# Kernel tuning notes

Hardware: AMD Instinct MI355X
Metric: run time of the kernel (lower is better)

Reference implementation:

```python
import jax
import jax.numpy as jnp
import numpy as np
from jax import lax

# Model dims (see init_kwargs)
B, C, D, M, L = 16, 64, 128, 16, 3
PROJ, OUT = 64, 1  # projection_size defaults to channels; output_size=1


def _spectral_conv(v, w1, w2, bias):
    """FNO 2D spectral convolution. v: [B,C,D,D]; w1,w2: [C,C,M,M,2] (re/im); bias: [C]."""
    vft = jnp.fft.rfft2(v, norm="backward")            # [B,C,D,D//2+1] complex
    w1c = w1[..., 0] + 1j * w1[..., 1]                   # [C,C,M,M]
    w2c = w2[..., 0] + 1j * w2[..., 1]
    top = jnp.einsum("bixy,ioxy->boxy", vft[:, :, :M, :M], w1c)
    bot = jnp.einsum("bixy,ioxy->boxy", vft[:, :, -M:, :M], w2c)
    out_ft = jnp.zeros_like(vft)
    out_ft = out_ft.at[:, :, :M, :M].set(top).at[:, :, -M:, :M].set(bot)
    out = jnp.fft.irfft2(out_ft, s=(D, D), norm="backward")
    return out + bias[None, :, None, None]               # in_bias


def _rk4(f, z0, ts):
    """Fixed-grid RK4 (torchdiffeq method='rk4'): one step per interval; return final state."""
    def step(z, tp):
        h = tp[1] - tp[0]
        k1 = f(z)
        k2 = f(z + 0.5 * h * k1)
        k3 = f(z + 0.5 * h * k2)
        k4 = f(z + h * k3)
        return z + (h / 6.0) * (k1 + 2.0 * k2 + 2.0 * k3 + k4), None
    pairs = jnp.stack([ts[:-1], ts[1:]], axis=1)         # [T-1, 2]
    zf, _ = lax.scan(step, z0, pairs)
    return zf


def setup_inputs() -> dict:
    key = jax.random.key(0)
    ks = jax.random.split(key, 12)
    scale = 1.0 / C                                       # FNO-style spectral weight scale
    z = jax.random.normal(ks[0], (B, 1, D, D), jnp.float32)
    lift_w = jax.random.normal(ks[1], (C, 1), jnp.float32)
    lift_b = jax.random.normal(ks[2], (C,), jnp.float32) * 0.1
    spec_w1 = jax.random.normal(ks[3], (L, C, C, M, M, 2), jnp.float32) * scale
    spec_w2 = jax.random.normal(ks[4], (L, C, C, M, M, 2), jnp.float32) * scale
    fl_bias = jax.random.normal(ks[5], (L, C), jnp.float32) * 0.1
    p1_w = jax.random.normal(ks[6], (PROJ, C), jnp.float32) / np.sqrt(C)
    p1_b = jax.random.normal(ks[7], (PROJ,), jnp.float32) * 0.1
    p2_w = jax.random.normal(ks[8], (OUT, PROJ), jnp.float32) / np.sqrt(PROJ)
    p2_b = jax.random.normal(ks[9], (OUT,), jnp.float32) * 0.1
    samp_ts = jnp.linspace(0.0, 1.0, 5, dtype=jnp.float32)
    return dict(z=z, lift_w=lift_w, lift_b=lift_b, spec_w1=spec_w1, spec_w2=spec_w2,
                fl_bias=fl_bias, p1_w=p1_w, p1_b=p1_b, p2_w=p2_w, p2_b=p2_b,
                samp_ts=samp_ts)


def reference(z, lift_w, lift_b, spec_w1, spec_w2, fl_bias, p1_w, p1_b, p2_w, p2_b, samp_ts):
    # Lifting: pointwise channel lift 1 -> C
    v = jnp.einsum("bixy,oi->boxy", z, lift_w) + lift_b[None, :, None, None]
    out = v
    # n_layers Fourier layers, each integrated with RK4 over samp_ts; take final time
    for l in range(L):
        f = lambda u, l=l: _spectral_conv(u, spec_w1[l], spec_w2[l], fl_bias[l])
        out = _rk4(f, out, samp_ts)
    # Projection: pointwise C -> PROJ -> OUT
    h = jnp.einsum("bcxy,pc->bpxy", out, p1_w) + p1_b[None, :, None, None]
    out = jnp.einsum("bpxy,op->boxy", h, p2_w) + p2_b[None, :, None, None]
    return out
```

## Files before the change

kernel.cpp:

```cpp
#include <hip/hip_runtime.h>

namespace {

constexpr int kNXI = 33;
constexpr int kNY = 16;
constexpr int kNMODE = kNY * kNXI;
constexpr int kModeBlocks = 529;
constexpr int kFwd1Blocks = 1024;

constexpr int WS_ALPHA = 0;
constexpr int WS_GAMMA = 1;
constexpr int WS_S = 4;
constexpr int WS_ZY = WS_S + kNMODE * 2;
constexpr int WS_T = WS_ZY;

constexpr float kTheta = 0.04908738521234052f;

__device__ __forceinline__ float wave_sum(float v) {
  v += __shfl_xor(v, 1);  v += __shfl_xor(v, 2);  v += __shfl_xor(v, 4);
  v += __shfl_xor(v, 8);  v += __shfl_xor(v, 16); v += __shfl_xor(v, 32);
  return v;
}

__global__ __launch_bounds__(256) void fnde_phase1(
    const float* __restrict__ w1, const float* __restrict__ w2,
    const float* __restrict__ flb, const float* __restrict__ lw,
    const float* __restrict__ lb, const float* __restrict__ ts,
    const float* __restrict__ p1w, const float* __restrict__ p1b,
    const float* __restrict__ p2w, const float* __restrict__ p2b,
    const float* __restrict__ z, float* __restrict__ ws) {
  const int b = blockIdx.x;
  const int t = threadIdx.x;

  if (b >= kModeBlocks) {
    __shared__ float zrow2[2][128], tcf[128], tsnf[128], rre2[2][128], rim2[2][128];
    const int bid = b - kModeBlocks;
    const int r = t >> 7, tt = t & 127;
    const int row = bid * 2 + r;
    const int bb = row >> 7, xs = row & 127;
    if (r == 0) sincosf((float)tt * kTheta, &tsnf[tt], &tcf[tt]);
    zrow2[r][tt] = z[bb * 16384 + xs * 128 + tt];
    __syncthreads();
    int y = tt & 15, part = tt >> 4;
    float sre = 0.f, sim = 0.f;
#pragma clang loop unroll(disable)
    for (int j = 0; j < 16; ++j) {
      int ys = (part << 4) + j;
      int k = (y * ys) & 127;
      float zv = zrow2[r][ys];
      sre += zv * tcf[k];
      sim -= zv * tsnf[k];
    }
    rre2[r][tt] = sre; rim2[r][tt] = sim;
    __syncthreads();
    if (tt < 16) {
      float ar = 0.f, ai = 0.f;
#pragma clang loop unroll(disable)
      for (int pp = 0; pp < 8; ++pp) { ar += rre2[r][(pp << 4) + tt]; ai += rim2[r][(pp << 4) + tt]; }
      int idx = (row * 16 + tt) * 2;
      ws[WS_ZY + idx] = ar; ws[WS_ZY + idx + 1] = ai;
    }
    return;
  }

  const int w = t >> 6, o = t & 63;
  const bool isBias = (b == kModeBlocks - 1);

  int xi = 0, y = 0, m = 0;
  if (!isBias) {
    const int xcd = b & 7, k = b >> 3;
    if (k < 64) { xi = xcd * 4 + (k >> 4); y = k & 15; }
    else        { xi = 32;                 y = xcd * 2 + (k - 64); }
    m = y * kNXI + xi;
    const bool inactive = (y == 0) ? (xi > 16) : (xi == 16);
    if (inactive) {
      if (t == 0) { ws[WS_S + 2 * m] = 0.f; ws[WS_S + 2 * m + 1] = 0.f; }
      return;
    }
  }

  __shared__ float2 ubuf[4][64];
  __shared__ float2 pbuf[2][4][64];

  float q = 0.f;
  if (w == 0) {
#pragma clang loop unroll(disable)
    for (int p = 0; p < 64; ++p) q = fmaf(p2w[p], p1w[p * 64 + o], q);
  }

  float zr = isBias ? lb[o] : lw[o], zi = 0.f;
  ubuf[w][o] = make_float2(zr, zi);

  int pb = 0;

#pragma clang loop unroll(disable)
  for (int l = 0; l < 3; ++l) {
    float2 Wc[16];
    if (isBias) {
      const float* lanep = w1 + o * 512;
#pragma unroll
      for (int j = 0; j < 16; ++j)
        Wc[j] = make_float2(lanep[(size_t)(l * 64 + 16 * w + j) * 32768], 0.f);
    } else if (y >= 1) {
      const float* lanep = ((xi <= 15) ? (w1 + (xi * 16 + y) * 2)
                                       : (w2 + ((xi - 17) * 16 + y) * 2)) + o * 512;
#pragma unroll
      for (int j = 0; j < 16; ++j)
        Wc[j] = *reinterpret_cast<const float2*>(
            lanep + (size_t)(l * 64 + 16 * w + j) * 32768);
    } else {
      const bool hasA = (xi <= 15);
      const float* lanepA = w1 + xi * 32 + o * 512;
      const float* lanepB = (xi >= 1) ? (w2 + (16 - xi) * 32 + o * 512)
                                      : (w1 + o * 512);
#pragma unroll
      for (int j = 0; j < 16; ++j) {
        const size_t ioff = (size_t)(l * 64 + 16 * w + j) * 32768;
        const float2 a = hasA ? *reinterpret_cast<const float2*>(lanepA + ioff)
                              : make_float2(0.f, 0.f);
        const float2 bb2 = *reinterpret_cast<const float2*>(lanepB + ioff);
        Wc[j] = make_float2(0.5f * (a.x + bb2.x), 0.5f * (a.y - bb2.y));
      }
    }
    const float bia = isBias ? flb[l * 64 + o] : 0.f;

#pragma clang loop unroll(disable)
    for (int step = 0; step < 4; ++step) {
      const float h = ts[step + 1] - ts[step];
      float accr = 0.f, acci = 0.f;
#pragma clang loop unroll(disable)
      for (int st = 0; st < 4; ++st) {
        float2 x[16];
#pragma unroll
        for (int jj = 0; jj < 8; ++jj)
          *reinterpret_cast<float4*>(&x[2 * jj]) =
              *reinterpret_cast<const float4*>(&ubuf[w][16 * w + 2 * jj]);
        float pr0 = 0.f, pi0 = 0.f, pr1 = 0.f, pi1 = 0.f;
#pragma unroll
        for (int j = 0; j < 16; j += 2) {
          pr0 = fmaf(Wc[j].x,     x[j].x,     pr0);  pr0 = fmaf(-Wc[j].y,     x[j].y,     pr0);
          pi0 = fmaf(Wc[j].x,     x[j].y,     pi0);  pi0 = fmaf(Wc[j].y,      x[j].x,     pi0);
          pr1 = fmaf(Wc[j + 1].x, x[j + 1].x, pr1);  pr1 = fmaf(-Wc[j + 1].y, x[j + 1].y, pr1);
          pi1 = fmaf(Wc[j + 1].x, x[j + 1].y, pi1);  pi1 = fmaf(Wc[j + 1].y,  x[j + 1].x, pi1);
        }
        pbuf[pb][w][o] = make_float2(pr0 + pr1, pi0 + pi1);
        __syncthreads();
        const float2 q0 = pbuf[pb][0][o], q1 = pbuf[pb][1][o];
        const float2 q2 = pbuf[pb][2][o], q3 = pbuf[pb][3][o];
        const float kr = q0.x + q1.x + q2.x + q3.x + bia;
        const float ki = q0.y + q1.y + q2.y + q3.y;
        const float wsm = (st == 1 || st == 2) ? 2.f : 1.f;
        accr = fmaf(wsm, kr, accr); acci = fmaf(wsm, ki, acci);
        float ur, ui;
        if (st < 3) {
          const float cm = (st < 2) ? 0.5f * h : h;
          ur = fmaf(cm, kr, zr); ui = fmaf(cm, ki, zi);
        } else {
          zr = fmaf(h * (1.f / 6.f), accr, zr);
          zi = fmaf(h * (1.f / 6.f), acci, zi);
          ur = zr; ui = zi;
        }
        ubuf[w][o] = make_float2(ur, ui);
        pb ^= 1;
      }
    }
  }

  if (w == 0) {
    if (isBias) {
      const float g = wave_sum(fmaf(p2w[o], p1b[o], q * zr));
      if (o == 0) ws[WS_GAMMA] = g + p2b[0];
    } else {
      const float sr = wave_sum(q * (zr - lw[o]));
      const float si = wave_sum(q * zi);
      if (o == 0) { ws[WS_S + 2 * m] = sr; ws[WS_S + 2 * m + 1] = si; }
      if (m == 0) {
        const float a = wave_sum(q * lw[o]);
        if (o == 0) ws[WS_ALPHA] = a;
      }
    }
  }
}

__global__ void fnde_mid(float* __restrict__ ws) {
  const int b = blockIdx.x >> 4, y = blockIdx.x & 15;
  const int t = threadIdx.x;
  __shared__ float cr[128], ci[128], tc[128], tsn[128], Sre[kNXI], Sim[kNXI];
  sincosf((float)t * kTheta, &tsn[t], &tc[t]);
  int idx = ((b * 128 + t) * 16 + y) * 2;
  cr[t] = ws[WS_ZY + idx]; ci[t] = ws[WS_ZY + idx + 1];
  __syncthreads();
  if (t < kNXI) {
    int x = (t <= 16) ? t : t + 95;
    float ar = 0.f, ai = 0.f;
    for (int xs = 0; xs < 128; ++xs) {
      int k = (x * xs) & 127;
      float c = tc[k], s = tsn[k];
      ar += cr[xs] * c + ci[xs] * s;
      ai += ci[xs] * c - cr[xs] * s;
    }
    int mm = y * kNXI + t;
    float sr = ws[WS_S + 2 * mm], si = ws[WS_S + 2 * mm + 1];
    Sre[t] = sr * ar - si * ai;
    Sim[t] = sr * ai + si * ar;
  }
  __syncthreads();
  const int xs = t;
  float ar, ai;
  if (y > 0) {
    ar = 0.f; ai = 0.f;
    for (int xj = 0; xj < kNXI; ++xj) {
      int x = (xj <= 16) ? xj : xj + 95;
      int k = (x * xs) & 127;
      float c = tc[k], s = tsn[k];
      ar += Sre[xj] * c - Sim[xj] * s;
      ai += Sre[xj] * s + Sim[xj] * c;
    }
  } else {
    ar = Sre[0]; ai = 0.f;
    for (int xj = 1; xj <= 16; ++xj) {
      int k = (xj * xs) & 127;
      ar += 2.f * (Sre[xj] * tc[k] - Sim[xj] * tsn[k]);
    }
  }
  ws[WS_T + idx] = ar; ws[WS_T + idx + 1] = ai;
}

__global__ void fnde_final(const float* __restrict__ z, const float* __restrict__ ws,
                           float* __restrict__ out) {
  const int bid = blockIdx.x;
  const int b = bid >> 7, xs = bid & 127;
  const int t = threadIdx.x;
  __shared__ float Tre[16], Tim[16], tc[128], tsn[128];
  sincosf((float)t * kTheta, &tsn[t], &tc[t]);
  if (t < 16) {
    int idx = ((b * 128 + xs) * 16 + t) * 2;
    Tre[t] = ws[WS_T + idx]; Tim[t] = ws[WS_T + idx + 1];
  }
  __syncthreads();
  float acc = Tre[0];
  for (int y = 1; y < 16; ++y) {
    int k = (y * t) & 127;
    acc += 2.f * (Tre[y] * tc[k] - Tim[y] * tsn[k]);
  }
  float val = ws[WS_ALPHA] * z[b * 16384 + xs * 128 + t] + ws[WS_GAMMA]
            + acc * (1.f / 16384.f);
  out[b * 16384 + xs * 128 + t] = val;
}

}

extern "C" void kernel_launch(void* const* d_in, const int* in_sizes, int n_in,
                              void* d_out, int out_size, void* d_ws, size_t ws_size,
                              hipStream_t stream) {
  (void)in_sizes; (void)n_in; (void)out_size; (void)ws_size;
  const float* z   = (const float*)d_in[0];
  const float* lw  = (const float*)d_in[1];
  const float* lb  = (const float*)d_in[2];
  const float* w1  = (const float*)d_in[3];
  const float* w2  = (const float*)d_in[4];
  const float* flb = (const float*)d_in[5];
  const float* p1w = (const float*)d_in[6];
  const float* p1b = (const float*)d_in[7];
  const float* p2w = (const float*)d_in[8];
  const float* p2b = (const float*)d_in[9];
  const float* ts  = (const float*)d_in[10];
  float* ws = (float*)d_ws;
  float* out = (float*)d_out;

  fnde_phase1<<<dim3(kModeBlocks + kFwd1Blocks), dim3(256), 0, stream>>>(
      w1, w2, flb, lw, lb, ts, p1w, p1b, p2w, p2b, z, ws);
  fnde_mid<<<dim3(256), dim3(128), 0, stream>>>(ws);
  fnde_final<<<dim3(2048), dim3(128), 0, stream>>>(z, ws, out);
}
```

Before: 97.09 us.

## Pack four modes per 512-thread block and broadcast state via readlane

Restructures the mode-integration blocks so each 512-thread block handles four modes, with two waves per mode each covering 32 input channels instead of four waves of 16. The per-stage shared-memory staging of the state vector is replaced by readlane broadcasts, and the forward row-DFT blocks now process four rows each. The aim is fewer blocks, fewer LDS round-trips and a cheaper reduction (two partials instead of four). In exchange, each thread holds 32 complex weights, which raises register pressure and may lower occupancy. Inactive modes now execute the full integration with dummy indices rather than exiting early.

```diff
diff --git a/kernel.cpp b/kernel.cpp
--- a/kernel.cpp
+++ b/kernel.cpp
@@ -3,10 +3,9 @@
 namespace {
 
 constexpr int kNXI = 33;
-constexpr int kNY = 16;
-constexpr int kNMODE = kNY * kNXI;
-constexpr int kModeBlocks = 529;
-constexpr int kFwd1Blocks = 1024;
+constexpr int kNMODE = 528;
+constexpr int kModeBlk = 133;
+constexpr int kFwd1Blk = 512;
 
 constexpr int WS_ALPHA = 0;
 constexpr int WS_GAMMA = 1;
@@ -16,13 +15,17 @@
 
 constexpr float kTheta = 0.04908738521234052f;
 
+__device__ __forceinline__ float rl(float v, int i) {
+  return __uint_as_float(__builtin_amdgcn_readlane(__float_as_uint(v), i));
+}
+
 __device__ __forceinline__ float wave_sum(float v) {
   v += __shfl_xor(v, 1);  v += __shfl_xor(v, 2);  v += __shfl_xor(v, 4);
   v += __shfl_xor(v, 8);  v += __shfl_xor(v, 16); v += __shfl_xor(v, 32);
   return v;
 }
 
-__global__ __launch_bounds__(256) void fnde_phase1(
+__global__ __launch_bounds__(512) void fnde_phase1(
     const float* __restrict__ w1, const float* __restrict__ w2,
     const float* __restrict__ flb, const float* __restrict__ lw,
     const float* __restrict__ lb, const float* __restrict__ ts,
@@ -32,126 +35,153 @@
   const int b = blockIdx.x;
   const int t = threadIdx.x;
 
-  if (b >= kModeBlocks) {
-    __shared__ float zrow2[2][128], tcf[128], tsnf[128], rre2[2][128], rim2[2][128];
-    const int bid = b - kModeBlocks;
+  if (b >= kModeBlk) {
+    __shared__ float zrow4[4][128], tcf[128], tsnf[128], rre4[4][128], rim4[4][128];
     const int r = t >> 7, tt = t & 127;
-    const int row = bid * 2 + r;
+    const int row = (b - kModeBlk) * 4 + r;
     const int bb = row >> 7, xs = row & 127;
     if (r == 0) sincosf((float)tt * kTheta, &tsnf[tt], &tcf[tt]);
-    zrow2[r][tt] = z[bb * 16384 + xs * 128 + tt];
+    zrow4[r][tt] = z[bb * 16384 + xs * 128 + tt];
     __syncthreads();
-    int y = tt & 15, part = tt >> 4;
+    const int y = tt & 15, part = tt >> 4;
     float sre = 0.f, sim = 0.f;
 #pragma clang loop unroll(disable)
     for (int j = 0; j < 16; ++j) {
-      int ys = (part << 4) + j;
-      int k = (y * ys) & 127;
-      float zv = zrow2[r][ys];
+      const int ys = (part << 4) + j;
+      const int k = (y * ys) & 127;
+      const float zv = zrow4[r][ys];
       sre += zv * tcf[k];
       sim -= zv * tsnf[k];
     }
-    rre2[r][tt] = sre; rim2[r][tt] = sim;
+    rre4[r][tt] = sre; rim4[r][tt] = sim;
     __syncthreads();
     if (tt < 16) {
       float ar = 0.f, ai = 0.f;
 #pragma clang loop unroll(disable)
-      for (int pp = 0; pp < 8; ++pp) { ar += rre2[r][(pp << 4) + tt]; ai += rim2[r][(pp << 4) + tt]; }
-      int idx = (row * 16 + tt) * 2;
+      for (int pp = 0; pp < 8; ++pp) { ar += rre4[r][(pp << 4) + tt]; ai += rim4[r][(pp << 4) + tt]; }
+      const int idx = (row * 16 + tt) * 2;
       ws[WS_ZY + idx] = ar; ws[WS_ZY + idx + 1] = ai;
     }
     return;
   }
 
-  const int w = t >> 6, o = t & 63;
-  const bool isBias = (b == kModeBlocks - 1);
-
-  int xi = 0, y = 0, m = 0;
-  if (!isBias) {
-    const int xcd = b & 7, k = b >> 3;
-    if (k < 64) { xi = xcd * 4 + (k >> 4); y = k & 15; }
-    else        { xi = 32;                 y = xcd * 2 + (k - 64); }
-    m = y * kNXI + xi;
-    const bool inactive = (y == 0) ? (xi > 16) : (xi == 16);
-    if (inactive) {
-      if (t == 0) { ws[WS_S + 2 * m] = 0.f; ws[WS_S + 2 * m + 1] = 0.f; }
-      return;
-    }
-  }
-
-  __shared__ float2 ubuf[4][64];
-  __shared__ float2 pbuf[2][4][64];
+  const int pp = t >> 7;
+  const int w = (t >> 6) & 1;
+  const int o = t & 63;
+  const int base = w * 32;
+  const bool isBiasBlk = (b == kModeBlk - 1);
+
+  __shared__ float2 pbuf[2][4][2][64];
+
+  const float t0 = ts[0], t1 = ts[1], t2 = ts[2], t3 = ts[3], t4 = ts[4];
+  const float h0 = t1 - t0, h1 = t2 - t1, h2 = t3 - t2, h3 = t4 - t3;
 
   float q = 0.f;
-  if (w == 0) {
-#pragma clang loop unroll(disable)
-    for (int p = 0; p < 64; ++p) q = fmaf(p2w[p], p1w[p * 64 + o], q);
-  }
-
-  float zr = isBias ? lb[o] : lw[o], zi = 0.f;
-  ubuf[w][o] = make_float2(zr, zi);
-
-  int pb = 0;
+#pragma clang loop unroll(disable)
+  for (int p = 0; p < 64; ++p) q = fmaf(p2w[p], p1w[p * 64 + o], q);
+
+  int pb = pp & 0;
+  pb = 0;
+
+  if (isBiasBlk) {
+    float e = lb[o];
+    const float* lanep = w1 + o * 512;
+#pragma clang loop unroll(disable)
+    for (int l = 0; l < 3; ++l) {
+      float Wr[32];
+#pragma unroll
+      for (int j = 0; j < 32; ++j)
+        Wr[j] = lanep[(size_t)(l * 64 + base + j) * 32768];
+      const float bia = flb[l * 64 + o];
+#pragma clang loop unroll(disable)
+      for (int step = 0; step < 4; ++step) {
+        const float h = (step == 0) ? h0 : (step == 1) ? h1 : (step == 2) ? h2 : h3;
+        float acc = 0.f;
+        float u = e;
+#pragma clang loop unroll(disable)
+        for (int st = 0; st < 4; ++st) {
+          float p0 = 0.f, p1 = 0.f;
+#pragma unroll
+          for (int j = 0; j < 32; j += 2) {
+            p0 = fmaf(Wr[j],     rl(u, base + j),     p0);
+            p1 = fmaf(Wr[j + 1], rl(u, base + j + 1), p1);
+          }
+          pbuf[pb][pp][w][o].x = p0 + p1;
+          __syncthreads();
+          const float kk = pbuf[pb][pp][0][o].x + pbuf[pb][pp][1][o].x + bia;
+          pb ^= 1;
+          const float wsm = (st == 1 || st == 2) ? 2.f : 1.f;
+          acc = fmaf(wsm, kk, acc);
+          if (st < 3) { const float cm = (st < 2) ? 0.5f * h : h; u = fmaf(cm, kk, e); }
+          else        { e = fmaf(h * (1.f / 6.f), acc, e); u = e; }
+        }
+      }
+    }
+    if (pp == 0 && w == 0) {
+      const float g = wave_sum(fmaf(p2w[o], p1b[o], q * e));
+      if (o == 0) ws[WS_GAMMA] = g + p2b[0];
+    }
+    return;
+  }
+
+  const int kk = b * 4 + pp;
+  const int xi = kk >> 4, y = kk & 15;
+  const int m = y * kNXI + xi;
+  const bool active = !((y == 0 && xi > 16) || (xi == 16 && y > 0));
+  const int xiE = active ? xi : 0;
+  const int yE = active ? y : 1;
+
+  float zr = lw[o], zi = 0.f;
+  float ur = zr, ui = zi;
 
 #pragma clang loop unroll(disable)
   for (int l = 0; l < 3; ++l) {
-    float2 Wc[16];
-    if (isBias) {
-      const float* lanep = w1 + o * 512;
-#pragma unroll
-      for (int j = 0; j < 16; ++j)
-        Wc[j] = make_float2(lanep[(size_t)(l * 64 + 16 * w + j) * 32768], 0.f);
-    } else if (y >= 1) {
-      const float* lanep = ((xi <= 15) ? (w1 + (xi * 16 + y) * 2)
-                                       : (w2 + ((xi - 17) * 16 + y) * 2)) + o * 512;
-#pragma unroll
-      for (int j = 0; j < 16; ++j)
-        Wc[j] = *reinterpret_cast<const float2*>(
-            lanep + (size_t)(l * 64 + 16 * w + j) * 32768);
+    float2 Wc[32];
+    if (yE >= 1) {
+      const float* lanep = ((xiE <= 15) ? (w1 + (xiE * 16 + yE) * 2)
+                                        : (w2 + ((xiE - 17) * 16 + yE) * 2)) + o * 512;
+#pragma unroll
+      for (int j = 0; j < 32; ++j)
+        Wc[j] = *reinterpret_cast<const float2*>(lanep + (size_t)(l * 64 + base + j) * 32768);
     } else {
-      const bool hasA = (xi <= 15);
-      const float* lanepA = w1 + xi * 32 + o * 512;
-      const float* lanepB = (xi >= 1) ? (w2 + (16 - xi) * 32 + o * 512)
-                                      : (w1 + o * 512);
-#pragma unroll
-      for (int j = 0; j < 16; ++j) {
-        const size_t ioff = (size_t)(l * 64 + 16 * w + j) * 32768;
+      const bool hasA = (xiE <= 15);
+      const float* lanepA = w1 + xiE * 32 + o * 512;
+      const float* lanepB = (xiE >= 1) ? (w2 + (16 - xiE) * 32 + o * 512)
+                                       : (w1 + o * 512);
+#pragma unroll
+      for (int j = 0; j < 32; ++j) {
+        const size_t ioff = (size_t)(l * 64 + base + j) * 32768;
         const float2 a = hasA ? *reinterpret_cast<const float2*>(lanepA + ioff)
                               : make_float2(0.f, 0.f);
         const float2 bb2 = *reinterpret_cast<const float2*>(lanepB + ioff);
         Wc[j] = make_float2(0.5f * (a.x + bb2.x), 0.5f * (a.y - bb2.y));
       }
     }
-    const float bia = isBias ? flb[l * 64 + o] : 0.f;
 
 #pragma clang loop unroll(disable)
     for (int step = 0; step < 4; ++step) {
-      const float h = ts[step + 1] - ts[step];
+      const float h = (step == 0) ? h0 : (step == 1) ? h1 : (step == 2) ? h2 : h3;
       float accr = 0.f, acci = 0.f;
 #pragma clang loop unroll(disable)
       for (int st = 0; st < 4; ++st) {
-        float2 x[16];
-#pragma unroll
-        for (int jj = 0; jj < 8; ++jj)
-          *reinterpret_cast<float4*>(&x[2 * jj]) =
-              *reinterpret_cast<const float4*>(&ubuf[w][16 * w + 2 * jj]);
         float pr0 = 0.f, pi0 = 0.f, pr1 = 0.f, pi1 = 0.f;
 #pragma unroll
-        for (int j = 0; j < 16; j += 2) {
-          pr0 = fmaf(Wc[j].x,     x[j].x,     pr0);  pr0 = fmaf(-Wc[j].y,     x[j].y,     pr0);
-          pi0 = fmaf(Wc[j].x,     x[j].y,     pi0);  pi0 = fmaf(Wc[j].y,      x[j].x,     pi0);
-          pr1 = fmaf(Wc[j + 1].x, x[j + 1].x, pr1);  pr1 = fmaf(-Wc[j + 1].y, x[j + 1].y, pr1);
-          pi1 = fmaf(Wc[j + 1].x, x[j + 1].y, pi1);  pi1 = fmaf(Wc[j + 1].y,  x[j + 1].x, pi1);
+        for (int j = 0; j < 32; j += 2) {
+          const float x0r = rl(ur, base + j),     x0i = rl(ui, base + j);
+          const float x1r = rl(ur, base + j + 1), x1i = rl(ui, base + j + 1);
+          pr0 = fmaf(Wc[j].x,     x0r, pr0);  pr0 = fmaf(-Wc[j].y,     x0i, pr0);
+          pi0 = fmaf(Wc[j].x,     x0i, pi0);  pi0 = fmaf(Wc[j].y,      x0r, pi0);
+          pr1 = fmaf(Wc[j + 1].x, x1r, pr1);  pr1 = fmaf(-Wc[j + 1].y, x1i, pr1);
+          pi1 = fmaf(Wc[j + 1].x, x1i, pi1);  pi1 = fmaf(Wc[j + 1].y,  x1r, pi1);
         }
-        pbuf[pb][w][o] = make_float2(pr0 + pr1, pi0 + pi1);
+        pbuf[pb][pp][w][o] = make_float2(pr0 + pr1, pi0 + pi1);
         __syncthreads();
-        const float2 q0 = pbuf[pb][0][o], q1 = pbuf[pb][1][o];
-        const float2 q2 = pbuf[pb][2][o], q3 = pbuf[pb][3][o];
-        const float kr = q0.x + q1.x + q2.x + q3.x + bia;
-        const float ki = q0.y + q1.y + q2.y + q3.y;
+        const float2 qa = pbuf[pb][pp][0][o], qb = pbuf[pb][pp][1][o];
+        pb ^= 1;
+        const float kr = qa.x + qb.x;
+        const float ki = qa.y + qb.y;
         const float wsm = (st == 1 || st == 2) ? 2.f : 1.f;
         accr = fmaf(wsm, kr, accr); acci = fmaf(wsm, ki, acci);
-        float ur, ui;
         if (st < 3) {
           const float cm = (st < 2) ? 0.5f * h : h;
           ur = fmaf(cm, kr, zr); ui = fmaf(cm, ki, zi);
@@ -160,17 +190,12 @@
           zi = fmaf(h * (1.f / 6.f), acci, zi);
           ur = zr; ui = zi;
         }
-        ubuf[w][o] = make_float2(ur, ui);
-        pb ^= 1;
       }
     }
   }
 
   if (w == 0) {
-    if (isBias) {
-      const float g = wave_sum(fmaf(p2w[o], p1b[o], q * zr));
-      if (o == 0) ws[WS_GAMMA] = g + p2b[0];
-    } else {
+    if (active) {
       const float sr = wave_sum(q * (zr - lw[o]));
       const float si = wave_sum(q * zi);
       if (o == 0) { ws[WS_S + 2 * m] = sr; ws[WS_S + 2 * m + 1] = si; }
@@ -178,6 +203,8 @@
         const float a = wave_sum(q * lw[o]);
         if (o == 0) ws[WS_ALPHA] = a;
       }
+    } else {
+      if (o == 0) { ws[WS_S + 2 * m] = 0.f; ws[WS_S + 2 * m + 1] = 0.f; }
     }
   }
 }
@@ -268,7 +295,7 @@
   float* ws = (float*)d_ws;
   float* out = (float*)d_out;
 
-  fnde_phase1<<<dim3(kModeBlocks + kFwd1Blocks), dim3(256), 0, stream>>>(
+  fnde_phase1<<<dim3(kModeBlk + kFwd1Blk), dim3(512), 0, stream>>>(
       w1, w2, flb, lw, lb, ts, p1w, p1b, p2w, p2b, z, ws);
   fnde_mid<<<dim3(256), dim3(128), 0, stream>>>(ws);
   fnde_final<<<dim3(2048), dim3(128), 0, stream>>>(z, ws, out);
```

Result: slower. 185.1 us (+90.6%).

## Split per-mode 3-layer RK4 chain into forward/adjoint halves meeting in the middle

Applied to the files above, without the earlier changes.

Each mode's serial chain of 12 RK4 steps (three layers of four) is split across two blocks. One block propagates the lifted vector forward through layers 0 and 1 (U). The other propagates the projection vector q backward through the transposed layer-2 operator (V). The scalar response is then recovered in the mid kernel as the dot product of V and U, and the bias/gamma term is handled by five small extra blocks. This halves the serial dependency length per block and doubles the block count. In exchange it adds workspace traffic, transposed (strided) weight loads, and redundant per-thread alpha and dot-product loops in the mid kernel.

```diff
diff --git a/kernel.cpp b/kernel.cpp
--- a/kernel.cpp
+++ b/kernel.cpp
@@ -3,38 +3,37 @@
 namespace {
 
 constexpr int kNXI = 33;
-constexpr int kNY = 16;
-constexpr int kNMODE = kNY * kNXI;
-constexpr int kModeBlocks = 529;
-constexpr int kFwd1Blocks = 1024;
-
-constexpr int WS_ALPHA = 0;
-constexpr int WS_GAMMA = 1;
-constexpr int WS_S = 4;
-constexpr int WS_ZY = WS_S + kNMODE * 2;
+constexpr int kNMODE = 528;
+constexpr int kChainBlk = 1061;
+constexpr int kFwd1Blk = 1024;
+
+constexpr int WS_Q = 0;
+constexpr int WS_GAMMA = 64;
+constexpr int WS_ALPHA = 65;
+constexpr int WS_G1 = 68;
+constexpr int WS_G2 = 132;
+constexpr int WS_G3 = 196;
+constexpr int WS_G4 = 260;
+constexpr int WS_G5 = 324;
+constexpr int WS_U = 392;
+constexpr int WS_V = WS_U + kNMODE * 128;
+constexpr int WS_ZY = WS_V + kNMODE * 128;
 constexpr int WS_T = WS_ZY;
 
 constexpr float kTheta = 0.04908738521234052f;
-
-__device__ __forceinline__ float wave_sum(float v) {
-  v += __shfl_xor(v, 1);  v += __shfl_xor(v, 2);  v += __shfl_xor(v, 4);
-  v += __shfl_xor(v, 8);  v += __shfl_xor(v, 16); v += __shfl_xor(v, 32);
-  return v;
-}
 
 __global__ __launch_bounds__(256) void fnde_phase1(
     const float* __restrict__ w1, const float* __restrict__ w2,
     const float* __restrict__ flb, const float* __restrict__ lw,
     const float* __restrict__ lb, const float* __restrict__ ts,
-    const float* __restrict__ p1w, const float* __restrict__ p1b,
-    const float* __restrict__ p2w, const float* __restrict__ p2b,
+    const float* __restrict__ p1w, const float* __restrict__ p2w,
     const float* __restrict__ z, float* __restrict__ ws) {
   const int b = blockIdx.x;
   const int t = threadIdx.x;
 
-  if (b >= kModeBlocks) {
+  if (b >= kChainBlk) {
     __shared__ float zrow2[2][128], tcf[128], tsnf[128], rre2[2][128], rim2[2][128];
-    const int bid = b - kModeBlocks;
+    const int bid = b - kChainBlk;
     const int r = t >> 7, tt = t & 127;
     const int row = bid * 2 + r;
     const int bb = row >> 7, xs = row & 127;
@@ -64,69 +63,89 @@
   }
 
   const int w = t >> 6, o = t & 63;
-  const bool isBias = (b == kModeBlocks - 1);
-
-  int xi = 0, y = 0, m = 0;
-  if (!isBias) {
-    const int xcd = b & 7, k = b >> 3;
+
+  int seg0L = 0, seg0N = 4, seg1L = 1, seg1N = 2;
+  int biasSeg = -1;
+  bool trans = false, herm = false, hasA = true, cplx = true;
+  bool needQ = false, writeQ = false, startLw = false, startLb = false;
+  const float* sA = w1;
+  const float* sB = w1;
+  int outOff = -1;
+
+  if (b < 1056) {
+    const int xcd = b & 7, kk = b >> 3;
+    const int k = kk >> 1, side = kk & 1;
+    int xi, y;
     if (k < 64) { xi = xcd * 4 + (k >> 4); y = k & 15; }
     else        { xi = 32;                 y = xcd * 2 + (k - 64); }
-    m = y * kNXI + xi;
+    const int m = y * kNXI + xi;
     const bool inactive = (y == 0) ? (xi > 16) : (xi == 16);
-    if (inactive) {
-      if (t == 0) { ws[WS_S + 2 * m] = 0.f; ws[WS_S + 2 * m + 1] = 0.f; }
-      return;
-    }
-  }
+    if (inactive) return;
+    herm = (y == 0);
+    if (!herm) {
+      sA = (xi <= 15) ? (w1 + (xi * 16 + y) * 2) : (w2 + ((xi - 17) * 16 + y) * 2);
+    } else {
+      hasA = (xi <= 15);
+      sA = w1 + xi * 32;
+      sB = (xi >= 1) ? (w2 + (16 - xi) * 32) : w1;
+    }
+    if (side == 0) { startLw = true;             outOff = WS_U + m * 128; }
+    else           { seg0L = 2; trans = true; needQ = true; outOff = WS_V + m * 128; }
+  } else {
+    const int g = b - 1056;
+    herm = true; hasA = true; sA = w1; sB = w1; cplx = false;
+    if      (g == 0) { startLb = true;                         outOff = WS_G1; }
+    else if (g == 1) { biasSeg = 0;                            outOff = WS_G2; }
+    else if (g == 2) { seg0L = 1; seg1N = 0; biasSeg = 0;      outOff = WS_G3; }
+    else if (g == 3) { seg0L = 2; seg1N = 0; biasSeg = 0;      outOff = WS_G4; }
+    else             { seg0L = 2; seg1N = 0; trans = true; needQ = true; writeQ = true;
+                       outOff = WS_G5; }
+  }
+
+  float qv = 0.f;
+  if (needQ) {
+#pragma clang loop unroll(disable)
+    for (int p = 0; p < 64; ++p) qv = fmaf(p2w[p], p1w[p * 64 + o], qv);
+  }
+  if (writeQ && w == 0) ws[WS_Q + o] = qv;
+
+  float zr = startLw ? lw[o] : startLb ? lb[o] : needQ ? qv : 0.f;
+  float zi = 0.f;
 
   __shared__ float2 ubuf[4][64];
   __shared__ float2 pbuf[2][4][64];
-
-  float q = 0.f;
-  if (w == 0) {
-#pragma clang loop unroll(disable)
-    for (int p = 0; p < 64; ++p) q = fmaf(p2w[p], p1w[p * 64 + o], q);
-  }
-
-  float zr = isBias ? lb[o] : lw[o], zi = 0.f;
   ubuf[w][o] = make_float2(zr, zi);
-
   int pb = 0;
 
-#pragma clang loop unroll(disable)
-  for (int l = 0; l < 3; ++l) {
+  const int segL[2] = {seg0L, seg1L};
+  const int segN[2] = {seg0N, seg1N};
+
+#pragma clang loop unroll(disable)
+  for (int sg = 0; sg < 2; ++sg) {
+    const int l = segL[sg], n = segN[sg];
+    if (n == 0) break;
     float2 Wc[16];
-    if (isBias) {
-      const float* lanep = w1 + o * 512;
 #pragma unroll
-      for (int j = 0; j < 16; ++j)
-        Wc[j] = make_float2(lanep[(size_t)(l * 64 + 16 * w + j) * 32768], 0.f);
-    } else if (y >= 1) {
-      const float* lanep = ((xi <= 15) ? (w1 + (xi * 16 + y) * 2)
-                                       : (w2 + ((xi - 17) * 16 + y) * 2)) + o * 512;
-#pragma unroll
-      for (int j = 0; j < 16; ++j)
-        Wc[j] = *reinterpret_cast<const float2*>(
-            lanep + (size_t)(l * 64 + 16 * w + j) * 32768);
-    } else {
-      const bool hasA = (xi <= 15);
-      const float* lanepA = w1 + xi * 32 + o * 512;
-      const float* lanepB = (xi >= 1) ? (w2 + (16 - xi) * 32 + o * 512)
-                                      : (w1 + o * 512);
-#pragma unroll
-      for (int j = 0; j < 16; ++j) {
-        const size_t ioff = (size_t)(l * 64 + 16 * w + j) * 32768;
-        const float2 a = hasA ? *reinterpret_cast<const float2*>(lanepA + ioff)
+    for (int j = 0; j < 16; ++j) {
+      const int v = 16 * w + j;
+      const size_t off = (size_t)l * 2097152 +
+          (trans ? ((size_t)o * 32768 + (size_t)v * 512)
+                 : ((size_t)v * 32768 + (size_t)o * 512));
+      if (!herm) {
+        Wc[j] = *reinterpret_cast<const float2*>(sA + off);
+      } else {
+        const float2 a = hasA ? *reinterpret_cast<const float2*>(sA + off)
                               : make_float2(0.f, 0.f);
-        const float2 bb2 = *reinterpret_cast<const float2*>(lanepB + ioff);
+        const float2 bb2 = *reinterpret_cast<const float2*>(sB + off);
         Wc[j] = make_float2(0.5f * (a.x + bb2.x), 0.5f * (a.y - bb2.y));
       }
     }
-    const float bia = isBias ? flb[l * 64 + o] : 0.f;
-
-#pragma clang loop unroll(disable)
-    for (int step = 0; step < 4; ++step) {
-      const float h = ts[step + 1] - ts[step];
+    const float bia = (biasSeg == sg) ? flb[l * 64 + o] : 0.f;
+
+#pragma clang loop unroll(disable)
+    for (int step = 0; step < n; ++step) {
+      const int si_ = trans ? (3 - step) : step;
+      const float h = ts[si_ + 1] - ts[si_];
       float accr = 0.f, acci = 0.f;
 #pragma clang loop unroll(disable)
       for (int st = 0; st < 4; ++st) {
@@ -167,28 +186,35 @@
   }
 
   if (w == 0) {
-    if (isBias) {
-      const float g = wave_sum(fmaf(p2w[o], p1b[o], q * zr));
-      if (o == 0) ws[WS_GAMMA] = g + p2b[0];
-    } else {
-      const float sr = wave_sum(q * (zr - lw[o]));
-      const float si = wave_sum(q * zi);
-      if (o == 0) { ws[WS_S + 2 * m] = sr; ws[WS_S + 2 * m + 1] = si; }
-      if (m == 0) {
-        const float a = wave_sum(q * lw[o]);
-        if (o == 0) ws[WS_ALPHA] = a;
-      }
-    }
-  }
-}
-
-__global__ void fnde_mid(float* __restrict__ ws) {
+    if (cplx) { ws[outOff + 2 * o] = zr; ws[outOff + 2 * o + 1] = zi; }
+    else      { ws[outOff + o] = zr; }
+  }
+}
+
+__global__ void fnde_mid(const float* __restrict__ lw, const float* __restrict__ p1b,
+                         const float* __restrict__ p2w, const float* __restrict__ p2b,
+                         float* __restrict__ ws) {
   const int b = blockIdx.x >> 4, y = blockIdx.x & 15;
   const int t = threadIdx.x;
   __shared__ float cr[128], ci[128], tc[128], tsn[128], Sre[kNXI], Sim[kNXI];
   sincosf((float)t * kTheta, &tsn[t], &tc[t]);
   int idx = ((b * 128 + t) * 16 + y) * 2;
   cr[t] = ws[WS_ZY + idx]; ci[t] = ws[WS_ZY + idx + 1];
+
+  if (blockIdx.x == 0 && t == 40) {
+    float g = p2b[0];
+    for (int p = 0; p < 64; ++p) g += p2w[p] * p1b[p];
+    for (int o = 0; o < 64; ++o) g += ws[WS_V + 2 * o] * ws[WS_G1 + o];
+    for (int o = 0; o < 64; ++o) g += ws[WS_V + 2 * o] * ws[WS_G2 + o];
+    for (int o = 0; o < 64; ++o) g += ws[WS_G5 + o] * ws[WS_G3 + o];
+    for (int o = 0; o < 64; ++o) g += ws[WS_Q + o] * ws[WS_G4 + o];
+    ws[WS_GAMMA] = g;
+  }
+  if (blockIdx.x == 0 && t == 41) {
+    float a = 0.f;
+    for (int p = 0; p < 64; ++p) a += ws[WS_Q + p] * lw[p];
+    ws[WS_ALPHA] = a;
+  }
   __syncthreads();
   if (t < kNXI) {
     int x = (t <= 16) ? t : t + 95;
@@ -199,8 +225,22 @@
       ar += cr[xs] * c + ci[xs] * s;
       ai += ci[xs] * c - cr[xs] * s;
     }
-    int mm = y * kNXI + t;
-    float sr = ws[WS_S + 2 * mm], si = ws[WS_S + 2 * mm + 1];
+    const int mm = y * kNXI + t;
+    const bool act = (y == 0) ? (t <= 16) : (t != 16);
+    float sr = 0.f, si = 0.f;
+    if (act) {
+      const float* up = ws + WS_U + mm * 128;
+      const float* vp = ws + WS_V + mm * 128;
+      float alpha = 0.f;
+      for (int p = 0; p < 64; ++p) alpha += ws[WS_Q + p] * lw[p];
+      for (int o = 0; o < 64; ++o) {
+        const float ur2 = up[2 * o], ui2 = up[2 * o + 1];
+        const float vr2 = vp[2 * o], vi2 = vp[2 * o + 1];
+        sr += vr2 * ur2 - vi2 * ui2;
+        si += vr2 * ui2 + vi2 * ur2;
+      }
+      sr -= alpha;
+    }
     Sre[t] = sr * ar - si * ai;
     Sim[t] = sr * ai + si * ar;
   }
@@ -268,8 +308,8 @@
   float* ws = (float*)d_ws;
   float* out = (float*)d_out;
 
-  fnde_phase1<<<dim3(kModeBlocks + kFwd1Blocks), dim3(256), 0, stream>>>(
-      w1, w2, flb, lw, lb, ts, p1w, p1b, p2w, p2b, z, ws);
-  fnde_mid<<<dim3(256), dim3(128), 0, stream>>>(ws);
+  fnde_phase1<<<dim3(kChainBlk + kFwd1Blk), dim3(256), 0, stream>>>(
+      w1, w2, flb, lw, lb, ts, p1w, p2w, z, ws);
+  fnde_mid<<<dim3(256), dim3(128), 0, stream>>>(lw, p1b, p2w, p2b, ws);
   fnde_final<<<dim3(2048), dim3(128), 0, stream>>>(z, ws, out);
 }
```

New measurement: 106.9 us. 1.1x slower.
